# Performance work log

Measured on AMD Instinct MI355X. Metric: run time of the kernel, lower is better.

Reference implementation:

```python
import jax, jax.numpy as jnp
import numpy as np
from math import sqrt

D_MODEL = 1024
D_HEAD = 128
TAU = 30.0
B, L = 8, 2048


def setup_inputs() -> dict:
    key = jax.random.key(0)
    k1, k2, k3, k4 = jax.random.split(key, 4)
    x = jax.random.normal(k1, (B, L, D_MODEL), dtype=jnp.float32)
    attention_mask = jnp.ones((B, L), dtype=jnp.int32)
    W_Q = jax.random.normal(k2, (D_HEAD, D_MODEL), dtype=jnp.float32)
    W_K = jax.random.normal(k3, (D_HEAD, D_MODEL), dtype=jnp.float32)
    W_V = jax.random.normal(k4, (D_HEAD, D_MODEL), dtype=jnp.float32)
    return {"input": x, "attention_mask": attention_mask, "W_Q": W_Q, "W_K": W_K, "W_V": W_V}


def reference(input, attention_mask, W_Q, W_K, W_V):
    # Single-head projections: [B, L, d_head]
    Q = input @ W_Q.T
    K = input @ W_K.T
    V = input @ W_V.T
    # Scaled scores: [B, L, L]
    S = jnp.einsum("bqd,bkd->bqk", Q, K) / sqrt(D_HEAD)
    # tanh soft-capping (mode == 'tanh-clipped')
    S = TAU * jnp.tanh(S)
    l = input.shape[1]
    # causal mask: strictly upper triangle -> -inf
    causal = jnp.triu(jnp.ones((l, l), dtype=bool), k=1)
    S = jnp.where(causal[None, :, :], -jnp.inf, S)
    # padding mask on keys: [B, 1, L]
    S = jnp.where(attention_mask[:, None, :] == 0, -jnp.inf, S)
    Attn = jax.nn.softmax(S, axis=-1)
    return Attn @ V
```

## Files before the change

kernel.cpp:

```cpp
#include <hip/hip_runtime.h>
#include <hip/hip_bf16.h>

#define BATCH  8
#define SEQ    2048
#define DMODEL 1024
#define DHEAD  128

typedef __attribute__((ext_vector_type(4))) float f32x4;
typedef __attribute__((ext_vector_type(4))) float f4;
typedef _Float16 f16;
typedef __attribute__((ext_vector_type(8))) _Float16 f16x8;
typedef __attribute__((ext_vector_type(8))) __bf16 bf16x8;
typedef __attribute__((ext_vector_type(16))) unsigned short u16x16;

__device__ __forceinline__ unsigned short f2bf(float f) {
    unsigned u = __builtin_bit_cast(unsigned, f);
    u += 0x7fffu + ((u >> 16) & 1u);
    return (unsigned short)(u >> 16);
}

#if __has_builtin(__builtin_amdgcn_exp2f)
#define EXP2(x) __builtin_amdgcn_exp2f(x)
#else
#define EXP2(x) exp2f(x)
#endif

__device__ __forceinline__ float fast_rcp(float x) {
#if __has_builtin(__builtin_amdgcn_rcpf)
    return __builtin_amdgcn_rcpf(x);
#else
    return 1.0f / x;
#endif
}

__global__ __launch_bounds__(256) void wsplit_kernel(
    const float* __restrict__ WQ, const float* __restrict__ WK,
    const float* __restrict__ WV, f16* __restrict__ Wsp)
{
    const int gid = blockIdx.x * 256 + threadIdx.x;
    const int row = gid & 127;
    const int hi  = (gid >> 7) & 3;
    const int ks  = (gid >> 9) & 31;
    const int mat = gid >> 14;
    const float* W = (mat < 2) ? WQ : (mat < 4) ? WK : WV;
    const float* src = W + (size_t)row * DMODEL + ks * 32 + hi * 8;
    f4 v0 = *(const f4*)src, v1 = *(const f4*)(src + 4);
    const bool lopart = (mat == 1 || mat == 3);
    f16x8 o;
    #pragma unroll
    for (int j = 0; j < 4; ++j) {
        f16 h0 = (f16)v0[j], h1 = (f16)v1[j];
        o[j]     = lopart ? (f16)(v0[j] - (float)h0) : h0;
        o[j + 4] = lopart ? (f16)(v1[j] - (float)h1) : h1;
    }
    *reinterpret_cast<f16x8*>(Wsp + (size_t)gid * 8) = o;
}

__global__ __launch_bounds__(256, 2) void proj_kernel(
    const float* __restrict__ x, const f16* __restrict__ Wsp,
    f16* __restrict__ Qh, f16* __restrict__ Ql,
    f16* __restrict__ Kh, f16* __restrict__ Kl,
    unsigned short* __restrict__ Vtb)
{
    __shared__ f16 Ax[2][2][4][4][17][8];

    const int tid  = threadIdx.x;
    const int lane = tid & 63;
    const int w    = tid >> 6;
    const int lo   = lane & 15;
    const int hi   = lane >> 4;
    const int m0   = blockIdx.x * 64;
    const int bn   = blockIdx.y;
    const int fi   = hi * 128 + bn * 64 + w * 16 + lo;

    const int xrow = tid >> 2;
    const int xg   = tid & 3;
    const int xrb  = xrow >> 4, xro = xrow & 15;

    f32x4 accQ[4] = {}, accK[4] = {}, accV[4] = {};

    const float* xbase = x + (size_t)(m0 + xrow) * DMODEL + xg * 8;
    const f16*   wbase = Wsp + (size_t)fi * 8;

    f4 rx0, rx1;
    auto loadX = [&](int ks) {
        rx0 = *(const f4*)(xbase + ks * 32);
        rx1 = *(const f4*)(xbase + ks * 32 + 4);
    };
    auto writeX = [&](int buf) {
        f16x8 h8, l8;
        #pragma unroll
        for (int j = 0; j < 4; ++j) {
            f16 h0 = (f16)rx0[j]; h8[j]     = h0; l8[j]     = (f16)(rx0[j] - (float)h0);
            f16 h1 = (f16)rx1[j]; h8[j + 4] = h1; l8[j + 4] = (f16)(rx1[j] - (float)h1);
        }
        *reinterpret_cast<f16x8*>(&Ax[buf][0][xrb][xg][xro][0]) = h8;
        *reinterpret_cast<f16x8*>(&Ax[buf][1][xrb][xg][xro][0]) = l8;
    };
    auto loadW = [&](int ks, f16x8 (&W5)[5]) {
        #pragma unroll
        for (int m = 0; m < 5; ++m)
            W5[m] = *reinterpret_cast<const f16x8*>(wbase + (size_t)(m * 32 + ks) * 4096);
    };
    auto STEP = [&](int ks, f16x8 (&Wc)[5], f16x8 (&Wn)[5]) {
        const int cur = ks & 1;
        if (ks < 31) { loadX(ks + 1); loadW(ks + 1, Wn); }
        #pragma unroll
        for (int rb = 0; rb < 4; ++rb) {
            f16x8 ah = *reinterpret_cast<const f16x8*>(&Ax[cur][0][rb][hi][lo][0]);
            f16x8 al = *reinterpret_cast<const f16x8*>(&Ax[cur][1][rb][hi][lo][0]);
            accQ[rb] = __builtin_amdgcn_mfma_f32_16x16x32_f16(ah, Wc[0], accQ[rb], 0, 0, 0);
            accQ[rb] = __builtin_amdgcn_mfma_f32_16x16x32_f16(ah, Wc[1], accQ[rb], 0, 0, 0);
            accQ[rb] = __builtin_amdgcn_mfma_f32_16x16x32_f16(al, Wc[0], accQ[rb], 0, 0, 0);
            accK[rb] = __builtin_amdgcn_mfma_f32_16x16x32_f16(ah, Wc[2], accK[rb], 0, 0, 0);
            accK[rb] = __builtin_amdgcn_mfma_f32_16x16x32_f16(ah, Wc[3], accK[rb], 0, 0, 0);
            accK[rb] = __builtin_amdgcn_mfma_f32_16x16x32_f16(al, Wc[2], accK[rb], 0, 0, 0);
            accV[rb] = __builtin_amdgcn_mfma_f32_16x16x32_f16(ah, Wc[4], accV[rb], 0, 0, 0);
        }
        if (ks < 31) writeX(cur ^ 1);
        __syncthreads();
    };

    f16x8 Wa[5], Wb[5];
    loadW(0, Wa);
    loadX(0);
    writeX(0);
    __syncthreads();

    for (int ks = 0; ks < 32; ks += 2) {
        STEP(ks,     Wa, Wb);
        STEP(ks + 1, Wb, Wa);
    }

    #pragma unroll
    for (int rb = 0; rb < 4; ++rb)
        #pragma unroll
        for (int r = 0; r < 4; ++r) {
            const int m = m0 + rb * 16 + hi * 4 + r;
            const int n = bn * 64 + w * 16 + lo;
            const size_t idx = (size_t)m * DHEAD + n;
            float vq = accQ[rb][r];
            f16 hq = (f16)vq;
            Qh[idx] = hq; Ql[idx] = (f16)(vq - (float)hq);
            float vk = accK[rb][r];
            f16 hk = (f16)vk;
            Kh[idx] = hk; Kl[idx] = (f16)(vk - (float)hk);
            const int bb = m >> 11, l = m & 2047;
            Vtb[((size_t)bb * DHEAD + n) * SEQ + l] = f2bf(accV[rb][r]);
        }
}

__global__ __launch_bounds__(512) void attn_kernel(
    const f16* __restrict__ Qh, const f16* __restrict__ Ql,
    const f16* __restrict__ Kh, const f16* __restrict__ Kl,
    const unsigned short* __restrict__ Vtb, const int* __restrict__ mask,
    float* __restrict__ out)
{
    __shared__ f16 Khs[2][64][136];
    __shared__ f16 Kls[2][64][136];
    __shared__ unsigned short Vs[2][128][72];
    __shared__ int Ms[2][64];
    __shared__ unsigned short Plds[8][16][40];

    const int tid  = threadIdx.x;
    const int lane = tid & 63;
    const int w    = tid >> 6;
    const int lo   = lane & 15;
    const int hi   = lane >> 4;
    const int wq   = w & 3;
    const int wk   = w >> 2;
    const int b    = blockIdx.x;
    const int qs   = 31 - (int)blockIdx.y;
    const int qrow = qs * 64 + wq * 16;
    const int niter = qs + 1;

    const float c2p = 0.25506061907448296f;
    const float c1  = -86.561702453337804f;

    f16x8 qh[4], ql[4];
    {
        const size_t off = ((size_t)(b * SEQ + qrow + lo)) * DHEAD + hi * 8;
        #pragma unroll
        for (int c = 0; c < 4; ++c) {
            qh[c] = *reinterpret_cast<const f16x8*>(Qh + off + c * 32);
            ql[c] = *reinterpret_cast<const f16x8*>(Ql + off + c * 32);
        }
    }

    const int krow = tid >> 3;
    const int kcol = (tid & 7) * 16;
    const int vrow = tid >> 2;
    const int vcol = (tid & 3) * 16;

    f16x8  rKh0, rKh1, rKl0, rKl1;
    u16x16 rV;
    int    rM = 0;

    auto load_tile = [&](int kb) {
        const size_t koff = ((size_t)(b * SEQ + kb + krow)) * DHEAD + kcol;
        rKh0 = *reinterpret_cast<const f16x8*>(Kh + koff);
        rKh1 = *reinterpret_cast<const f16x8*>(Kh + koff + 8);
        rKl0 = *reinterpret_cast<const f16x8*>(Kl + koff);
        rKl1 = *reinterpret_cast<const f16x8*>(Kl + koff + 8);
        rV   = *reinterpret_cast<const u16x16*>(Vtb + ((size_t)b * DHEAD + vrow) * SEQ + kb + vcol);
        if (tid < 64) rM = mask[b * SEQ + kb + tid];
    };
    auto write_tile = [&](int buf) {
        *reinterpret_cast<f16x8*>(&Khs[buf][krow][kcol])     = rKh0;
        *reinterpret_cast<f16x8*>(&Khs[buf][krow][kcol + 8]) = rKh1;
        *reinterpret_cast<f16x8*>(&Kls[buf][krow][kcol])     = rKl0;
        *reinterpret_cast<f16x8*>(&Kls[buf][krow][kcol + 8]) = rKl1;
        *reinterpret_cast<u16x16*>(&Vs[buf][vrow][vcol]) = rV;
        if (tid < 64) Ms[buf][tid] = rM;
    };

    load_tile(0);
    write_tile(0);
    __syncthreads();

    f32x4 acc[8] = {};
    float rs[4] = {0.f, 0.f, 0.f, 0.f};

    for (int it = 0; it < niter; ++it) {
        const int cur = it & 1;
        if (it + 1 < niter) load_tile((it + 1) * 64);

        const int kb = it * 64 + wk * 32;
        if (kb <= qrow + 15) {
            #pragma unroll
            for (int h = 0; h < 2; ++h) {
                f32x4 s = {};
                #pragma unroll
                for (int c = 0; c < 4; ++c) {
                    f16x8 fkh = *reinterpret_cast<const f16x8*>(&Khs[cur][wk * 32 + h * 16 + lo][c * 32 + hi * 8]);
                    f16x8 fkl = *reinterpret_cast<const f16x8*>(&Kls[cur][wk * 32 + h * 16 + lo][c * 32 + hi * 8]);
                    s = __builtin_amdgcn_mfma_f32_16x16x32_f16(qh[c], fkh, s, 0, 0, 0);
                    s = __builtin_amdgcn_mfma_f32_16x16x32_f16(qh[c], fkl, s, 0, 0, 0);
                    s = __builtin_amdgcn_mfma_f32_16x16x32_f16(ql[c], fkh, s, 0, 0, 0);
                }
                const int key = kb + h * 16 + lo;
                const int mk  = Ms[cur][wk * 32 + h * 16 + lo];
                #pragma unroll
                for (int r = 0; r < 4; ++r) {
                    const int q = qrow + hi * 4 + r;
                    float t = EXP2(s[r] * c2p);
                    float p = EXP2(c1 * fast_rcp(t + 1.0f));
                    p = (key <= q && mk != 0) ? p : 0.0f;
                    rs[r] += p;
                    Plds[w][hi * 4 + r][h * 16 + lo] = f2bf(p);
                }
            }
            bf16x8 pa = *reinterpret_cast<const bf16x8*>(&Plds[w][lo][hi * 8]);
            #pragma unroll
            for (int dt = 0; dt < 8; ++dt) {
                bf16x8 vf = *reinterpret_cast<const bf16x8*>(&Vs[cur][dt * 16 + lo][wk * 32 + hi * 8]);
                acc[dt] = __builtin_amdgcn_mfma_f32_16x16x32_bf16(pa, vf, acc[dt], 0, 0, 0);
            }
        }

        if (it + 1 < niter) write_tile(cur ^ 1);
        __syncthreads();
    }

    float* red = (float*)&Khs[0][0][0];
    if (wk == 1) {
        float* dst = red + ((size_t)wq * 64 + lane) * 36;
        #pragma unroll
        for (int dt = 0; dt < 8; ++dt)
            #pragma unroll
            for (int r = 0; r < 4; ++r) dst[dt * 4 + r] = acc[dt][r];
        #pragma unroll
        for (int r = 0; r < 4; ++r) dst[32 + r] = rs[r];
    }
    __syncthreads();
    if (wk == 0) {
        const float* src = red + ((size_t)wq * 64 + lane) * 36;
        #pragma unroll
        for (int dt = 0; dt < 8; ++dt)
            #pragma unroll
            for (int r = 0; r < 4; ++r) acc[dt][r] += src[dt * 4 + r];
        float inv[4];
        #pragma unroll
        for (int r = 0; r < 4; ++r) {
            float v = rs[r] + src[32 + r];
            v += __shfl_xor(v, 1);
            v += __shfl_xor(v, 2);
            v += __shfl_xor(v, 4);
            v += __shfl_xor(v, 8);
            inv[r] = fast_rcp(v);
        }
        #pragma unroll
        for (int dt = 0; dt < 8; ++dt)
            #pragma unroll
            for (int r = 0; r < 4; ++r) {
                const size_t q = (size_t)qrow + hi * 4 + r;
                out[((size_t)b * SEQ + q) * DHEAD + dt * 16 + lo] = acc[dt][r] * inv[r];
            }
    }
}

extern "C" void kernel_launch(void* const* d_in, const int* in_sizes, int n_in,
                              void* d_out, int out_size, void* d_ws, size_t ws_size,
                              hipStream_t stream) {
    const float* x   = (const float*)d_in[0];
    const int*   msk = (const int*)d_in[1];
    const float* WQ  = (const float*)d_in[2];
    const float* WK  = (const float*)d_in[3];
    const float* WV  = (const float*)d_in[4];
    float* out = (float*)d_out;

    const size_t NE = (size_t)BATCH * SEQ * DHEAD;
    f16* Qh = (f16*)d_ws;
    f16* Ql = Qh + NE;
    f16* Kh = Ql + NE;
    f16* Kl = Kh + NE;
    unsigned short* Vtb = (unsigned short*)(Kl + NE);
    f16* Wsp = (f16*)(Vtb + NE);

    wsplit_kernel<<<320, 256, 0, stream>>>(WQ, WK, WV, Wsp);
    proj_kernel<<<dim3(BATCH * SEQ / 64, 2), 256, 0, stream>>>(x, Wsp, Qh, Ql, Kh, Kl, Vtb);
    attn_kernel<<<dim3(BATCH, 32), 512, 0, stream>>>(Qh, Ql, Kh, Kl, Vtb, msk, out);
}
```

Measured before the change: 102.2 us.

## Split attention key loop across two blocks with partial-sum merge kernel

Each attention block's key tiles are divided between two blocks along a new grid z dimension, each taking every other tile. Each block writes unnormalized partial outputs and row sums to workspace, and a new merge kernel adds the two halves and normalizes. The aim is to double the grid from 256 blocks so more compute units stay busy and the long causal rows finish sooner. The cost is an extra launch and a round trip of partial results through global memory.

```diff
diff --git a/kernel.cpp b/kernel.cpp
--- a/kernel.cpp
+++ b/kernel.cpp
@@ -150,11 +150,12 @@
         }
 }
 
+#define PART_STRIDE 8256
 __global__ __launch_bounds__(512) void attn_kernel(
     const f16* __restrict__ Qh, const f16* __restrict__ Ql,
     const f16* __restrict__ Kh, const f16* __restrict__ Kl,
     const unsigned short* __restrict__ Vtb, const int* __restrict__ mask,
-    float* __restrict__ out)
+    float* __restrict__ part)
 {
     __shared__ f16 Khs[2][64][136];
     __shared__ f16 Kls[2][64][136];
@@ -171,8 +172,8 @@
     const int wk   = w >> 2;
     const int b    = blockIdx.x;
     const int qs   = 31 - (int)blockIdx.y;
+    const int z    = blockIdx.z;
     const int qrow = qs * 64 + wq * 16;
-    const int niter = qs + 1;
 
     const float c2p = 0.25506061907448296f;
     const float c1  = -86.561702453337804f;
@@ -214,16 +215,18 @@
         if (tid < 64) Ms[buf][tid] = rM;
     };
 
-    load_tile(0);
+    load_tile(z * 64);
     write_tile(0);
     __syncthreads();
 
     f32x4 acc[8] = {};
     float rs[4] = {0.f, 0.f, 0.f, 0.f};
 
-    for (int it = 0; it < niter; ++it) {
-        const int cur = it & 1;
-        if (it + 1 < niter) load_tile((it + 1) * 64);
+    int cnt = 0;
+    for (int it = z; it <= qs; it += 2, ++cnt) {
+        const int cur = cnt & 1;
+        const bool havenext = (it + 2 <= qs);
+        if (havenext) load_tile((it + 2) * 64);
 
         const int kb = it * 64 + wk * 32;
         if (kb <= qrow + 15) {
@@ -258,7 +261,7 @@
             }
         }
 
-        if (it + 1 < niter) write_tile(cur ^ 1);
+        if (havenext) write_tile(cur ^ 1);
         __syncthreads();
     }
 
@@ -279,7 +282,7 @@
         for (int dt = 0; dt < 8; ++dt)
             #pragma unroll
             for (int r = 0; r < 4; ++r) acc[dt][r] += src[dt * 4 + r];
-        float inv[4];
+        float rsum[4];
         #pragma unroll
         for (int r = 0; r < 4; ++r) {
             float v = rs[r] + src[32 + r];
@@ -287,16 +290,38 @@
             v += __shfl_xor(v, 2);
             v += __shfl_xor(v, 4);
             v += __shfl_xor(v, 8);
-            inv[r] = fast_rcp(v);
-        }
+            rsum[r] = v;
+        }
+        float* P = part + (((size_t)b * 32 + qs) * 2 + z) * PART_STRIDE;
         #pragma unroll
         for (int dt = 0; dt < 8; ++dt)
             #pragma unroll
-            for (int r = 0; r < 4; ++r) {
-                const size_t q = (size_t)qrow + hi * 4 + r;
-                out[((size_t)b * SEQ + q) * DHEAD + dt * 16 + lo] = acc[dt][r] * inv[r];
-            }
-    }
+            for (int r = 0; r < 4; ++r)
+                P[(wq * 16 + hi * 4 + r) * 128 + dt * 16 + lo] = acc[dt][r];
+        if (lo == 0)
+            #pragma unroll
+            for (int r = 0; r < 4; ++r)
+                P[8192 + wq * 16 + hi * 4 + r] = rsum[r];
+    }
+}
+
+__global__ __launch_bounds__(256) void merge_kernel(
+    const float* __restrict__ part, float* __restrict__ out)
+{
+    const int gid = blockIdx.x * 256 + threadIdx.x;
+    const int col = (gid & 31) * 4;
+    const int q   = gid >> 5;
+    const int b   = q >> 11, l = q & 2047;
+    const int qs  = l >> 6, row = l & 63;
+    const float* P0 = part + (((size_t)b * 32 + qs) * 2) * PART_STRIDE;
+    const float* P1 = P0 + PART_STRIDE;
+    f4 a0 = *(const f4*)(P0 + row * 128 + col);
+    f4 a1 = *(const f4*)(P1 + row * 128 + col);
+    float inv = fast_rcp(P0[8192 + row] + P1[8192 + row]);
+    f4 o;
+    #pragma unroll
+    for (int j = 0; j < 4; ++j) o[j] = (a0[j] + a1[j]) * inv;
+    *(f4*)(out + (size_t)q * 128 + col) = o;
 }
 
 extern "C" void kernel_launch(void* const* d_in, const int* in_sizes, int n_in,
@@ -316,8 +341,10 @@
     f16* Kl = Kh + NE;
     unsigned short* Vtb = (unsigned short*)(Kl + NE);
     f16* Wsp = (f16*)(Vtb + NE);
+    float* part = (float*)(Wsp + (size_t)5 * 32 * 4096);
 
     wsplit_kernel<<<320, 256, 0, stream>>>(WQ, WK, WV, Wsp);
     proj_kernel<<<dim3(BATCH * SEQ / 64, 2), 256, 0, stream>>>(x, Wsp, Qh, Ql, Kh, Kl, Vtb);
-    attn_kernel<<<dim3(BATCH, 32), 512, 0, stream>>>(Qh, Ql, Kh, Kl, Vtb, msk, out);
-}
+    attn_kernel<<<dim3(BATCH, 32, 2), 512, 0, stream>>>(Qh, Ql, Kh, Kl, Vtb, msk, part);
+    merge_kernel<<<2048, 256, 0, stream>>>(part, out);
+}
```

Result: faster. 90.10 us (-11.8%).
